# Performance work log

Hardware: AMD Instinct MI355X
Metric: run time of the kernel (lower is better)

Reference implementation:

```python
import jax, jax.numpy as jnp
import numpy as np
from jax import lax

MAX_INT = 10000.0
V, T0, E, H = 100000, 20, 256, 256
T = T0 + 2          # tagset_size + 2 (start = T-2, stop = T-1)
B, S = 32, 512
H2 = H // 2


def setup_inputs() -> dict:
    key = jax.random.key(0)
    ks = jax.random.split(key, 18)
    sd = 0.08
    trans = jax.random.normal(ks[0], (T, T), jnp.float32)
    trans = trans.at[-2, :].set(-MAX_INT).at[:, -1].set(-MAX_INT)
    return {
        "X": jax.random.randint(ks[1], (B, S), 0, V, jnp.int64),
        "Y": jax.random.randint(ks[2], (B, S), 0, T0, jnp.int64),
        "emb": jax.random.normal(ks[3], (V, E), jnp.float32) * sd,
        "Wih_f": jax.random.normal(ks[4], (4 * H2, E), jnp.float32) * sd,
        "Whh_f": jax.random.normal(ks[5], (4 * H2, H2), jnp.float32) * sd,
        "bih_f": jax.random.normal(ks[6], (4 * H2,), jnp.float32) * sd,
        "bhh_f": jax.random.normal(ks[7], (4 * H2,), jnp.float32) * sd,
        "Wih_b": jax.random.normal(ks[8], (4 * H2, E), jnp.float32) * sd,
        "Whh_b": jax.random.normal(ks[9], (4 * H2, H2), jnp.float32) * sd,
        "bih_b": jax.random.normal(ks[10], (4 * H2,), jnp.float32) * sd,
        "bhh_b": jax.random.normal(ks[11], (4 * H2,), jnp.float32) * sd,
        "fcW": jax.random.normal(ks[12], (T, H), jnp.float32) * sd,
        "fcb": jax.random.normal(ks[13], (T,), jnp.float32) * sd,
        "trans": trans,
        # original draws random (h0, c0) of shape (2, seq_len, H//2) each call
        "h0": jax.random.normal(ks[14], (2, S, H2), jnp.float32),
        "c0": jax.random.normal(ks[15], (2, S, H2), jnp.float32),
    }


def _lstm_dir(x, h0, c0, Wih, Whh, bih, bhh, reverse):
    # x: [B, S, E]; scans over axis 0 (as torch LSTM with batch_first=False does here)
    def step(carry, xt):
        h, c = carry
        g = xt @ Wih.T + bih + h @ Whh.T + bhh          # [S, 4*H2]
        i, f, gg, o = jnp.split(g, 4, axis=-1)
        c2 = jax.nn.sigmoid(f) * c + jax.nn.sigmoid(i) * jnp.tanh(gg)
        h2 = jax.nn.sigmoid(o) * jnp.tanh(c2)
        return (h2, c2), h2
    xs = x[::-1] if reverse else x
    _, hs = lax.scan(step, (h0, c0), xs)
    return hs[::-1] if reverse else hs                  # [B, S, H2]


def _feats(X, emb, Wih_f, Whh_f, bih_f, bhh_f, Wih_b, Whh_b, bih_b, bhh_b,
           fcW, fcb, h0, c0):
    e = emb[X]                                           # [B, S, E]
    hf = _lstm_dir(e, h0[0], c0[0], Wih_f, Whh_f, bih_f, bhh_f, False)
    hb = _lstm_dir(e, h0[1], c0[1], Wih_b, Whh_b, bih_b, bhh_b, True)
    lstm_out = jnp.concatenate([hf, hb], axis=-1)        # [B, S, H]
    return lstm_out @ fcW.T + fcb                        # [B, S, T]


def _crf_loss(feats, Y, trans):
    # forward algorithm (log partition), vectorized over batch
    alpha0 = jnp.full((B, T), -MAX_INT, feats.dtype).at[:, -2].set(0.0)

    def step(alpha, feat_t):                             # feat_t: [B, T]
        # alpha_new[b, next] = LSE_prev(alpha[b,prev] + trans[next,prev]) + feat[b,next]
        new = jax.nn.logsumexp(alpha[:, None, :] + trans[None, :, :], axis=2) + feat_t
        return new, None

    alpha, _ = lax.scan(step, alpha0, jnp.swapaxes(feats, 0, 1))
    forward_score = jax.nn.logsumexp(alpha + trans[-1][None, :], axis=1).mean()

    # gold score
    start = jnp.full((B, 1), T - 2, Y.dtype)
    tags = jnp.concatenate([start, Y], axis=1)           # [B, S+1]
    emit = jnp.take_along_axis(feats, Y[..., None], axis=2)[..., 0].sum(axis=1)
    trans_sc = trans[tags[:, 1:], tags[:, :-1]].sum(axis=1) + trans[-1, tags[:, -1]]
    gold_score = (emit + trans_sc).mean()
    return forward_score - gold_score


def reference(X, Y, emb, Wih_f, Whh_f, bih_f, bhh_f, Wih_b, Whh_b, bih_b, bhh_b,
              fcW, fcb, trans, h0, c0):
    feats = _feats(X, emb, Wih_f, Whh_f, bih_f, bhh_f, Wih_b, Whh_b, bih_b, bhh_b,
                   fcW, fcb, h0, c0)
    score = _crf_loss(feats, Y, trans)
    return score, Y
```

## Files before the change

### kernel.cpp

```cpp
#include <hip/hip_runtime.h>
#include <hip/hip_bf16.h>
#include <stdint.h>

typedef __attribute__((ext_vector_type(8))) short short8;
typedef __attribute__((ext_vector_type(4))) float f32x4;
typedef __attribute__((ext_vector_type(4))) unsigned short ushort4v;

#define NB 32
#define NS 512
#define NE 256
#define NH2 128
#define NG 512
#define NT 22

__device__ __forceinline__ unsigned short f2bf(float f) {
    union { float f; unsigned u; } v; v.f = f;
    unsigned r = v.u + 0x7fffu + ((v.u >> 16) & 1u);
    return (unsigned short)(r >> 16);
}
__device__ __forceinline__ float bf2f(unsigned short b) {
    union { unsigned u; float f; } v; v.u = ((unsigned)b) << 16;
    return v.f;
}
__device__ __forceinline__ float sigmoidf_(float x) {
    return __builtin_amdgcn_rcpf(1.f + __expf(-x));
}
__device__ __forceinline__ float tanhf_(float x) {
    return 1.f - 2.f * __builtin_amdgcn_rcpf(__expf(2.f * x) + 1.f);
}
__device__ __forceinline__ void wg_barrier() {
    __builtin_amdgcn_sched_barrier(0);
    asm volatile("s_waitcnt lgkmcnt(0)" ::: "memory");
    __builtin_amdgcn_s_barrier();
    __builtin_amdgcn_sched_barrier(0);
}
#define GL16(gsrc, ldst)                                                              \
    __builtin_amdgcn_global_load_lds(                                                 \
        (const __attribute__((address_space(1))) unsigned int*)(gsrc),                \
        (__attribute__((address_space(3))) unsigned int*)(ldst), 16, 0, 0)

__global__ void k_pre(const int* X, const float* emb, const int* Y,
                      const float* Wih_f, const float* Wih_b,
                      const float* Whh_f, const float* Whh_b, const float* fcW,
                      unsigned short* ebf, unsigned short* Wb_ih,
                      unsigned short* Wb_hh, unsigned short* fcpad, float* out)
{
    int idx = blockIdx.x * blockDim.x + threadIdx.x;
    const int nEmb = NB * NS * 64;
    if (idx < nEmb) {
        int r = idx >> 6, lane = idx & 63;
        int xr = X[r];
        f32x4 v = *(const f32x4*)(emb + (size_t)xr * NE + lane * 4);
        ushort4v o;
        o[0] = f2bf(v[0]); o[1] = f2bf(v[1]); o[2] = f2bf(v[2]); o[3] = f2bf(v[3]);
        *(ushort4v*)(ebf + (size_t)r * NE + lane * 4) = o;
        return;
    }
    int j = idx - nEmb;
    const int n1 = 2 * NG * NE;
    const int n2 = 2 * NG * NH2;
    const int n3 = 2 * 32 * NH2;
    const int n4 = NB * NS;
    if (j < n1) {
        const float* src = (j < NG * NE) ? Wih_f : Wih_b;
        Wb_ih[j] = f2bf(src[j % (NG * NE)]);
    } else if (j < n1 + n2) {
        int i2 = j - n1;
        const float* src = (i2 < NG * NH2) ? Whh_f : Whh_b;
        Wb_hh[i2] = f2bf(src[i2 % (NG * NH2)]);
    } else if (j < n1 + n2 + n3) {
        int i3 = j - n1 - n2;
        int d = i3 / (32 * NH2);
        int jj = (i3 / NH2) % 32;
        int k = i3 % NH2;
        fcpad[i3] = (jj < NT) ? f2bf(fcW[jj * 256 + d * NH2 + k]) : (unsigned short)0;
    } else if (j < n1 + n2 + n3 + n4) {
        int i4 = j - n1 - n2 - n3;
        out[1 + i4] = (float)Y[i4];
    }
}

__launch_bounds__(256)
__global__ void k_xproj(const unsigned short* ebf, const unsigned short* Wb_ih,
                        const float* bih_f, const float* bhh_f,
                        const float* bih_b, const float* bhh_b,
                        unsigned short* Xp)
{
    __shared__ __align__(16) unsigned short Atile[128 * 64];
    __shared__ __align__(16) unsigned short Btile[128 * 64];
    int dir = blockIdx.z;
    int r0 = blockIdx.x * 128;
    int g0 = blockIdx.y * 128;
    int tid = threadIdx.x;
    int w = tid >> 6, lane = tid & 63;
    int wr = w >> 1, wc = w & 1;
    int lrow = lane & 15, kg = lane >> 4;
    int srow8 = lane >> 3, schunk = lane & 7;
    const float* bih = dir ? bih_b : bih_f;
    const float* bhh = dir ? bhh_b : bhh_f;
    const unsigned short* Bsrc = Wb_ih + ((size_t)dir * NG + g0) * NE;
    const unsigned short* Asrc = ebf + (size_t)r0 * NE;

    f32x4 acc[4][4] = {};
#pragma unroll
    for (int ks = 0; ks < 4; ++ks) {
        int k0 = ks * 64;
#pragma unroll
        for (int i = 0; i < 4; ++i) {
            int rr = (w * 4 + i) * 8 + srow8;
            GL16(Asrc + (size_t)rr * NE + k0 + schunk * 8, Atile + (w * 4 + i) * 512);
            GL16(Bsrc + (size_t)rr * NE + k0 + schunk * 8, Btile + (w * 4 + i) * 512);
        }
        __syncthreads();
        short8 a[4][2], b[4][2];
#pragma unroll
        for (int mi = 0; mi < 4; ++mi)
#pragma unroll
            for (int kk = 0; kk < 2; ++kk)
                a[mi][kk] = *(const short8*)&Atile[(wr * 64 + mi * 16 + lrow) * 64 + kk * 32 + kg * 8];
#pragma unroll
        for (int ni = 0; ni < 4; ++ni)
#pragma unroll
            for (int kk = 0; kk < 2; ++kk)
                b[ni][kk] = *(const short8*)&Btile[(wc * 64 + ni * 16 + lrow) * 64 + kk * 32 + kg * 8];
#pragma unroll
        for (int mi = 0; mi < 4; ++mi)
#pragma unroll
            for (int ni = 0; ni < 4; ++ni)
#pragma unroll
                for (int kk = 0; kk < 2; ++kk)
                    acc[mi][ni] = __builtin_amdgcn_mfma_f32_16x16x32_bf16(a[mi][kk], b[ni][kk], acc[mi][ni], 0, 0, 0);
        __syncthreads();
    }

#pragma unroll
    for (int ni = 0; ni < 4; ++ni) {
        int g = g0 + wc * 64 + ni * 16 + lrow;
        float bias = bih[g] + bhh[g];
#pragma unroll
        for (int mi = 0; mi < 4; ++mi) {
            int r = r0 + wr * 64 + mi * 16 + kg * 4;
            int t = r >> 9;
            int s = r & 511;
            int sb = s >> 4;
            unsigned short* dst = Xp + ((((size_t)dir * 32 + sb) * 32 + t) << 13) + g * 16 + (s & 15);
            unsigned o0 = f2bf(acc[mi][ni][0] + bias);
            unsigned o1 = f2bf(acc[mi][ni][1] + bias);
            unsigned o2 = f2bf(acc[mi][ni][2] + bias);
            unsigned o3 = f2bf(acc[mi][ni][3] + bias);
            uint2 pk; pk.x = o0 | (o1 << 16); pk.y = o2 | (o3 << 16);
            *(uint2*)dst = pk;
        }
    }
}

__launch_bounds__(512, 2)
__global__ void k_lstm(const unsigned short* Wb_hh, const unsigned short* Xp,
                       unsigned short* Hout, const float* h0, const float* c0)
{
    __shared__ unsigned short h_lds[2][16 * 136];
    int dir = blockIdx.x >> 5;
    int sb = blockIdx.x & 31;
    int s0 = sb * 16;
    int tid = threadIdx.x;
    int w = tid >> 6, lane = tid & 63;
    int lrow = lane & 15, kg = lane >> 4;

    short8 bfr[4][4];
#pragma unroll
    for (int q = 0; q < 4; ++q) {
        const unsigned short* p = Wb_hh + ((size_t)dir * NG + (q * 128 + w * 16 + lrow)) * NH2 + kg * 8;
#pragma unroll
        for (int kf = 0; kf < 4; ++kf)
            bfr[q][kf] = *(const short8*)(p + kf * 32);
    }

    float c[4];
#pragma unroll
    for (int i = 0; i < 4; ++i)
        c[i] = c0[((size_t)dir * NS + s0 + kg * 4 + i) * NH2 + w * 16 + lrow];
    {
        int sl = tid >> 5, hq = tid & 31;
        f32x4 hv = *(const f32x4*)(h0 + ((size_t)dir * NS + s0 + sl) * NH2 + hq * 4);
        ushort4v hb; hb[0] = f2bf(hv[0]); hb[1] = f2bf(hv[1]); hb[2] = f2bf(hv[2]); hb[3] = f2bf(hv[3]);
        *(ushort4v*)&h_lds[0][sl * 136 + hq * 4] = hb;
    }

    const unsigned short* xbase = Xp + (((size_t)dir * 32 + sb) * 32) * 8192;
    unsigned short* hslot = Hout + (((size_t)dir * 32 + sb) * 32) * 2048;
    int xoff0 = (w * 16 + lrow) * 16 + kg * 4;

    ushort4v xA[4], xB[4];
#pragma unroll
    for (int q = 0; q < 4; ++q)
        xA[q] = *(const ushort4v*)(xbase + (size_t)(dir ? 31 : 0) * 8192 + xoff0 + q * 2048);
#pragma unroll
    for (int q = 0; q < 4; ++q)
        xB[q] = *(const ushort4v*)(xbase + (size_t)(dir ? 30 : 1) * 8192 + xoff0 + q * 2048);
    __syncthreads();

#define LSTM_STEP(T, XV, PR, PW)                                                       \
    {                                                                                  \
        int tx = dir ? 31 - (T) : (T);                                                 \
        short8 afr[4];                                                                 \
        _Pragma("unroll")                                                              \
        for (int kf = 0; kf < 4; ++kf)                                                 \
            afr[kf] = *(const short8*)&h_lds[PR][lrow * 136 + kf * 32 + kg * 8];       \
        f32x4 acc[4] = {};                                                             \
        _Pragma("unroll")                                                              \
        for (int q = 0; q < 4; ++q)                                                    \
            _Pragma("unroll")                                                          \
            for (int kf = 0; kf < 4; ++kf)                                             \
                acc[q] = __builtin_amdgcn_mfma_f32_16x16x32_bf16(afr[kf], bfr[q][kf],  \
                                                                 acc[q], 0, 0, 0);     \
        float gs[4][4];                                                                \
        _Pragma("unroll")                                                              \
        for (int q = 0; q < 4; ++q)                                                    \
            _Pragma("unroll")                                                          \
            for (int i = 0; i < 4; ++i)                                                \
                gs[q][i] = acc[q][i] + bf2f(XV[q][i]);                                 \
        if ((T) + 2 < 32) {                                                            \
            int txn = dir ? 29 - (T) : (T) + 2;                                        \
            _Pragma("unroll")                                                          \
            for (int q = 0; q < 4; ++q)                                                \
                XV[q] = *(const ushort4v*)(xbase + (size_t)txn * 8192 + xoff0 + q * 2048); \
        }                                                                              \
        _Pragma("unroll")                                                              \
        for (int i = 0; i < 4; ++i) {                                                  \
            float ci = sigmoidf_(gs[1][i]) * c[i] + sigmoidf_(gs[0][i]) * tanhf_(gs[2][i]); \
            c[i] = ci;                                                                 \
            unsigned short hb = f2bf(sigmoidf_(gs[3][i]) * tanhf_(ci));                \
            h_lds[PW][(kg * 4 + i) * 136 + w * 16 + lrow] = hb;                        \
            hslot[(size_t)tx * 2048 + (kg * 4 + i) * 128 + w * 16 + lrow] = hb;        \
        }                                                                              \
        wg_barrier();                                                                  \
    }

    for (int tt = 0; tt < 16; ++tt) {
        LSTM_STEP(2 * tt,     xA, ((2 * tt) & 1),     (((2 * tt) & 1) ^ 1))
        LSTM_STEP(2 * tt + 1, xB, ((2 * tt + 1) & 1), (((2 * tt + 1) & 1) ^ 1))
    }
#undef LSTM_STEP
}

__device__ __forceinline__ float mm_combine(const unsigned short* Rb, const unsigned short* Tb,
                                            int lane, f32x4 c[2][2])
{
    int lrow = lane & 15, kg = lane >> 4;
    short8 a0 = *(const short8*)(Rb + lrow * 32 + kg * 8);
    short8 a1 = *(const short8*)(Rb + (16 + lrow) * 32 + kg * 8);
    short8 b0 = *(const short8*)(Tb + lrow * 32 + kg * 8);
    short8 b1 = *(const short8*)(Tb + (16 + lrow) * 32 + kg * 8);
    c[0][0] = __builtin_amdgcn_mfma_f32_16x16x32_bf16(a0, b0, c[0][0], 0, 0, 0);
    c[0][1] = __builtin_amdgcn_mfma_f32_16x16x32_bf16(a0, b1, c[0][1], 0, 0, 0);
    c[1][0] = __builtin_amdgcn_mfma_f32_16x16x32_bf16(a1, b0, c[1][0], 0, 0, 0);
    c[1][1] = __builtin_amdgcn_mfma_f32_16x16x32_bf16(a1, b1, c[1][1], 0, 0, 0);
    float mx = 0.f;
#pragma unroll
    for (int ti = 0; ti < 2; ++ti)
#pragma unroll
        for (int tj = 0; tj < 2; ++tj)
#pragma unroll
            for (int i = 0; i < 4; ++i) mx = fmaxf(mx, c[ti][tj][i]);
#pragma unroll
    for (int off = 32; off; off >>= 1) mx = fmaxf(mx, __shfl_xor(mx, off));
    return fmaxf(mx, 1e-30f);
}

__device__ __forceinline__ void write_scaled(unsigned short* outp, bool Rlayout,
                                             int lane, const f32x4 c[2][2], float inv)
{
    int lrow = lane & 15, kg = lane >> 4;
    if (Rlayout) {
#pragma unroll
        for (int ti = 0; ti < 2; ++ti)
#pragma unroll
            for (int tj = 0; tj < 2; ++tj) {
                int cc = tj * 16 + lrow;
#pragma unroll
                for (int i = 0; i < 4; ++i) {
                    int r = ti * 16 + kg * 4 + i;
                    float v = (r < NT && cc < NT) ? c[ti][tj][i] * inv : 0.f;
                    outp[r * 32 + cc] = f2bf(v);
                }
            }
    } else {
#pragma unroll
        for (int ti = 0; ti < 2; ++ti)
#pragma unroll
            for (int tj = 0; tj < 2; ++tj) {
                int cc = tj * 16 + lrow;
                int r0 = ti * 16 + kg * 4;
                ushort4v pk;
#pragma unroll
                for (int i = 0; i < 4; ++i) {
                    int r = r0 + i;
                    float v = (r < NT && cc < NT) ? c[ti][tj][i] * inv : 0.f;
                    pk[i] = f2bf(v);
                }
                *(ushort4v*)(outp + cc * 32 + r0) = pk;
            }
    }
}

__launch_bounds__(256)
__global__ void k_fcrf(const unsigned short* Hout, const unsigned short* fcpad,
                       const float* fcb, const float* trans,
                       float* feats, unsigned short* Mseg, float* lscseg)
{
    __shared__ unsigned short mats[16 * 1024];
    __shared__ float etR[484], etT[484];
    __shared__ float ef[16 * 24];
    __shared__ float lscm[16];
    __shared__ f32x4 part[2][64];
    int b = blockIdx.x, seg = blockIdx.y;
    int tid = threadIdx.x;
    int w = tid >> 6, lane = tid & 63;
    int lrow = lane & 15, kg = lane >> 4;

    f32x4 fa[2] = {};
    if (w < 2) {
        int dir = w;
        const unsigned short* hb = Hout + (((size_t)dir * 32 + seg) * 32 + b) * 2048 + lrow * 128 + kg * 8;
        const unsigned short* fb = fcpad + dir * 4096 + lrow * 128 + kg * 8;
#pragma unroll
        for (int kf = 0; kf < 4; ++kf) {
            short8 a  = *(const short8*)(hb + kf * 32);
            short8 b0 = *(const short8*)(fb + kf * 32);
            short8 b1 = *(const short8*)(fb + 2048 + kf * 32);
            fa[0] = __builtin_amdgcn_mfma_f32_16x16x32_bf16(a, b0, fa[0], 0, 0, 0);
            fa[1] = __builtin_amdgcn_mfma_f32_16x16x32_bf16(a, b1, fa[1], 0, 0, 0);
        }
        if (dir == 1) { part[0][lane] = fa[0]; part[1][lane] = fa[1]; }
        if (w == 1 && lane < 16) lscm[lane] = 0.f;
    } else {
        for (int i = tid - 128; i < 484; i += 128) {
            float e = __expf(trans[i]);
            etR[i] = e;
            etT[(i % NT) * NT + (i / NT)] = e;
        }
    }
    __syncthreads();
    if (w == 0) {
        fa[0] += part[0][lane];
        fa[1] += part[1][lane];
#pragma unroll
        for (int nf = 0; nf < 2; ++nf) {
            int tag = nf * 16 + lrow;
            if (tag < NT) {
                float bias = fcb[tag];
#pragma unroll
                for (int i = 0; i < 4; ++i) {
                    int s = kg * 4 + i;
                    float f = fa[nf][i] + bias;
                    feats[((size_t)b * NS + seg * 16 + s) * NT + tag] = f;
                    ef[s * 24 + tag] = __expf(f);
                }
            }
        }
    }
    __syncthreads();

    for (int idx = tid; idx < 16 * 1024; idx += 256) {
        int t = idx >> 10, cell = idx & 1023, row = cell >> 5, col = cell & 31;
        float v = 0.f;
        if (row < NT && col < NT) {
            v = (t & 1) ? etR[row * NT + col] * ef[t * 24 + row]
                        : etT[row * NT + col] * ef[t * 24 + col];
        }
        mats[idx] = f2bf(v);
    }
    __syncthreads();

    for (int lvl = 0; lvl < 4; ++lvl) {
        int nP = 8 >> lvl;
        for (int p = w; p < nP; p += 4) {
            int aslot = (2 * p) << lvl, bslot = (2 * p + 1) << lvl;
            f32x4 c[2][2] = {};
            float mx = mm_combine(mats + bslot * 1024, mats + aslot * 1024, lane, c);
            float inv = __builtin_amdgcn_rcpf(mx);
            float nlsc = lscm[aslot] + lscm[bslot] + __logf(mx);
            if (lvl < 3) {
                write_scaled(mats + aslot * 1024, (p & 1) != 0, lane, c, inv);
                if (lane == 0) lscm[aslot] = nlsc;
            } else {
                write_scaled(Mseg + ((size_t)b * 32 + seg) * 1024, (seg & 1) != 0, lane, c, inv);
                if (lane == 0) lscseg[b * 32 + seg] = nlsc;
            }
        }
        __syncthreads();
    }
}

__launch_bounds__(256)
__global__ void k_crf2(const unsigned short* Mseg, const float* lscseg,
                       const float* feats, const float* trans, const int* Y,
                       float* fwd_sc, float* gold_sc)
{
    __shared__ unsigned short mats[16 * 1024];
    __shared__ float lscm[16];
    __shared__ float tl[484];
    __shared__ float col20[32];
    __shared__ float red[4];
    int b = blockIdx.x;
    int tid = threadIdx.x;
    int w = tid >> 6, lane = tid & 63;
    int lrow = lane & 15, kg = lane >> 4;

    for (int i = tid; i < 484; i += 256) tl[i] = trans[i];
    __syncthreads();

    const unsigned short* base = Mseg + (size_t)b * 32 * 1024;
    for (int p = w; p < 16; p += 4) {
        f32x4 c[2][2] = {};
        float mx = mm_combine(base + (2 * p + 1) * 1024, base + (2 * p) * 1024, lane, c);
        float inv = __builtin_amdgcn_rcpf(mx);
        float nlsc = lscseg[b * 32 + 2 * p] + lscseg[b * 32 + 2 * p + 1] + __logf(mx);
        write_scaled(mats + p * 1024, (p & 1) != 0, lane, c, inv);
        if (lane == 0) lscm[p] = nlsc;
    }
    __syncthreads();

    for (int lvl = 0; lvl < 4; ++lvl) {
        int nP = 8 >> lvl;
        for (int p = w; p < nP; p += 4) {
            int aslot = (2 * p) << lvl, bslot = (2 * p + 1) << lvl;
            f32x4 c[2][2] = {};
            float mx = mm_combine(mats + bslot * 1024, mats + aslot * 1024, lane, c);
            if (lvl < 3) {
                float inv = __builtin_amdgcn_rcpf(mx);
                float nlsc = lscm[aslot] + lscm[bslot] + __logf(mx);
                write_scaled(mats + aslot * 1024, (p & 1) != 0, lane, c, inv);
                if (lane == 0) lscm[aslot] = nlsc;
            } else {
                if (lrow == 4) {
#pragma unroll
                    for (int ti = 0; ti < 2; ++ti)
#pragma unroll
                        for (int i = 0; i < 4; ++i)
                            col20[ti * 16 + kg * 4 + i] = c[ti][1][i];
                }
                if (lane == 0) lscm[0] = lscm[0] + lscm[8];
            }
        }
        __syncthreads();
    }

    if (w == 0) {
        float v = 0.f;
        if (lane < NT) v = __expf(tl[(NT - 1) * NT + lane]) * col20[lane];
#pragma unroll
        for (int off = 32; off; off >>= 1) v += __shfl_xor(v, off);
        if (lane == 0) fwd_sc[b] = __logf(v) + lscm[0];
    }

    const float* fb = feats + (size_t)b * NS * NT;
    float acc = 0.f;
    for (int s = tid; s < NS; s += 256) {
        int y = Y[b * NS + s];
        int yp = s ? Y[b * NS + s - 1] : (NT - 2);
        acc += fb[s * NT + y] + tl[y * NT + yp];
    }
    if (tid == 0) acc += tl[(NT - 1) * NT + Y[b * NS + NS - 1]];
#pragma unroll
    for (int off = 32; off; off >>= 1) acc += __shfl_xor(acc, off);
    if (lane == 0) red[w] = acc;
    __syncthreads();
    if (tid == 0) gold_sc[b] = red[0] + red[1] + red[2] + red[3];
}

__global__ void k_final(const float* fwd_sc, const float* gold_sc, float* out)
{
    float v = (threadIdx.x < NB) ? (fwd_sc[threadIdx.x] - gold_sc[threadIdx.x]) : 0.f;
#pragma unroll
    for (int off = 32; off; off >>= 1) v += __shfl_xor(v, off);
    if (threadIdx.x == 0) out[0] = v * (1.f / NB);
}

extern "C" void kernel_launch(void* const* d_in, const int* in_sizes, int n_in,
                              void* d_out, int out_size, void* d_ws, size_t ws_size,
                              hipStream_t stream)
{
    const int* X = (const int*)d_in[0];
    const int* Y = (const int*)d_in[1];
    const float* emb = (const float*)d_in[2];
    const float* Wih_f = (const float*)d_in[3];
    const float* Whh_f = (const float*)d_in[4];
    const float* bih_f = (const float*)d_in[5];
    const float* bhh_f = (const float*)d_in[6];
    const float* Wih_b = (const float*)d_in[7];
    const float* Whh_b = (const float*)d_in[8];
    const float* bih_b = (const float*)d_in[9];
    const float* bhh_b = (const float*)d_in[10];
    const float* fcW = (const float*)d_in[11];
    const float* fcb = (const float*)d_in[12];
    const float* trans = (const float*)d_in[13];
    const float* h0 = (const float*)d_in[14];
    const float* c0 = (const float*)d_in[15];
    float* out = (float*)d_out;

    char* ws = (char*)d_ws;
    unsigned short* Wb_ih = (unsigned short*)(ws + 0);
    unsigned short* Wb_hh = (unsigned short*)(ws + 524288);
    unsigned short* fcpad = (unsigned short*)(ws + 786432);
    unsigned short* Xp    = (unsigned short*)(ws + 802816);
    float* feats          = (float*)(ws + 34357248);
    float* fwd_sc         = (float*)(ws + 35799040);
    float* gold_sc        = (float*)(ws + 35799168);
    unsigned short* ebf   = (unsigned short*)(ws + 35799296);
    unsigned short* Mseg  = ebf;
    float* lscseg         = (float*)(ws + 35799296 + 2097152);
    unsigned short* Hout  = (unsigned short*)(ws + 44187904);

    k_pre<<<dim3(5728), dim3(256), 0, stream>>>(X, emb, Y, Wih_f, Wih_b, Whh_f, Whh_b,
                                                fcW, ebf, Wb_ih, Wb_hh, fcpad, out);
    k_xproj<<<dim3(128, 4, 2), dim3(256), 0, stream>>>(ebf, Wb_ih, bih_f, bhh_f, bih_b, bhh_b, Xp);
    k_lstm<<<dim3(64), dim3(512), 0, stream>>>(Wb_hh, Xp, Hout, h0, c0);
    k_fcrf<<<dim3(32, 32), dim3(256), 0, stream>>>(Hout, fcpad, fcb, trans, feats, Mseg, lscseg);
    k_crf2<<<dim3(NB), dim3(256), 0, stream>>>(Mseg, lscseg, feats, trans, Y, fwd_sc, gold_sc);
    k_final<<<dim3(1), dim3(64), 0, stream>>>(fwd_sc, gold_sc, out);
    (void)in_sizes; (void)n_in; (void)out_size; (void)ws_size;
}
```

Measured before the change: 97.65 us.

## Fuse FC projection into LSTM recurrence and double-buffer input projection GEMM

The LSTM kernel now computes the FC tag projection of each previous hidden state with extra MFMAs inside the recurrence and stages per-direction partial features in LDS. It then writes them out instead of storing the full hidden sequence to global memory. The FC/CRF kernel sums the two direction partials plus bias and computes per-segment gold-score partials, so k_crf2 only reduces them. The xproj GEMM gains double-buffered LDS tiles with explicit waitcnt/barrier scheduling to overlap loads with MFMA. The cost is extra MFMA and LDS work on the serial LSTM critical path for two of the waves.

```diff
diff --git a/kernel.cpp b/kernel.cpp
--- a/kernel.cpp
+++ b/kernel.cpp
@@ -86,8 +86,8 @@
                         const float* bih_b, const float* bhh_b,
                         unsigned short* Xp)
 {
-    __shared__ __align__(16) unsigned short Atile[128 * 64];
-    __shared__ __align__(16) unsigned short Btile[128 * 64];
+    __shared__ __align__(16) unsigned short Atile[2][128 * 64];
+    __shared__ __align__(16) unsigned short Btile[2][128 * 64];
     int dir = blockIdx.z;
     int r0 = blockIdx.x * 128;
     int g0 = blockIdx.y * 128;
@@ -101,28 +101,42 @@
     const unsigned short* Bsrc = Wb_ih + ((size_t)dir * NG + g0) * NE;
     const unsigned short* Asrc = ebf + (size_t)r0 * NE;
 
+#define STAGE(bufi, ks)                                                                \
+    do {                                                                               \
+        int k0_ = (ks) * 64;                                                           \
+        _Pragma("unroll")                                                              \
+        for (int i_ = 0; i_ < 4; ++i_) {                                               \
+            int rr_ = (w * 4 + i_) * 8 + srow8;                                        \
+            GL16(Asrc + (size_t)rr_ * NE + k0_ + schunk * 8, &Atile[bufi][(w * 4 + i_) * 512]); \
+            GL16(Bsrc + (size_t)rr_ * NE + k0_ + schunk * 8, &Btile[bufi][(w * 4 + i_) * 512]); \
+        }                                                                              \
+    } while (0)
+
+    STAGE(0, 0);
     f32x4 acc[4][4] = {};
 #pragma unroll
     for (int ks = 0; ks < 4; ++ks) {
-        int k0 = ks * 64;
-#pragma unroll
-        for (int i = 0; i < 4; ++i) {
-            int rr = (w * 4 + i) * 8 + srow8;
-            GL16(Asrc + (size_t)rr * NE + k0 + schunk * 8, Atile + (w * 4 + i) * 512);
-            GL16(Bsrc + (size_t)rr * NE + k0 + schunk * 8, Btile + (w * 4 + i) * 512);
+        const int cur = ks & 1;
+        if (ks < 3) {
+            STAGE(cur ^ 1, ks + 1);
+            asm volatile("s_waitcnt vmcnt(8)" ::: "memory");
+        } else {
+            asm volatile("s_waitcnt vmcnt(0)" ::: "memory");
         }
-        __syncthreads();
+        __builtin_amdgcn_sched_barrier(0);
+        __builtin_amdgcn_s_barrier();
+        __builtin_amdgcn_sched_barrier(0);
         short8 a[4][2], b[4][2];
 #pragma unroll
         for (int mi = 0; mi < 4; ++mi)
 #pragma unroll
             for (int kk = 0; kk < 2; ++kk)
-                a[mi][kk] = *(const short8*)&Atile[(wr * 64 + mi * 16 + lrow) * 64 + kk * 32 + kg * 8];
+                a[mi][kk] = *(const short8*)&Atile[cur][(wr * 64 + mi * 16 + lrow) * 64 + kk * 32 + kg * 8];
 #pragma unroll
         for (int ni = 0; ni < 4; ++ni)
 #pragma unroll
             for (int kk = 0; kk < 2; ++kk)
-                b[ni][kk] = *(const short8*)&Btile[(wc * 64 + ni * 16 + lrow) * 64 + kk * 32 + kg * 8];
+                b[ni][kk] = *(const short8*)&Btile[cur][(wc * 64 + ni * 16 + lrow) * 64 + kk * 32 + kg * 8];
 #pragma unroll
         for (int mi = 0; mi < 4; ++mi)
 #pragma unroll
@@ -130,8 +144,12 @@
 #pragma unroll
                 for (int kk = 0; kk < 2; ++kk)
                     acc[mi][ni] = __builtin_amdgcn_mfma_f32_16x16x32_bf16(a[mi][kk], b[ni][kk], acc[mi][ni], 0, 0, 0);
-        __syncthreads();
-    }
+        asm volatile("s_waitcnt lgkmcnt(0)" ::: "memory");
+        __builtin_amdgcn_sched_barrier(0);
+        __builtin_amdgcn_s_barrier();
+        __builtin_amdgcn_sched_barrier(0);
+    }
+#undef STAGE
 
 #pragma unroll
     for (int ni = 0; ni < 4; ++ni) {
@@ -155,10 +173,12 @@
 }
 
 __launch_bounds__(512, 2)
-__global__ void k_lstm(const unsigned short* Wb_hh, const unsigned short* Xp,
-                       unsigned short* Hout, const float* h0, const float* c0)
+__global__ void k_lstm(const unsigned short* Wb_hh, const unsigned short* fcpad,
+                       const unsigned short* Xp, const float* h0, const float* c0,
+                       float* featsP)
 {
     __shared__ unsigned short h_lds[2][16 * 136];
+    __shared__ float featsL[32 * 16 * 24];
     int dir = blockIdx.x >> 5;
     int sb = blockIdx.x & 31;
     int s0 = sb * 16;
@@ -173,6 +193,13 @@
 #pragma unroll
         for (int kf = 0; kf < 4; ++kf)
             bfr[q][kf] = *(const short8*)(p + kf * 32);
+    }
+    short8 fcfr[4];
+    if (w < 2) {
+        const unsigned short* p = fcpad + ((size_t)dir * 32 + (w * 16 + lrow)) * NH2 + kg * 8;
+#pragma unroll
+        for (int kf = 0; kf < 4; ++kf)
+            fcfr[kf] = *(const short8*)(p + kf * 32);
     }
 
     float c[4];
@@ -187,9 +214,7 @@
     }
 
     const unsigned short* xbase = Xp + (((size_t)dir * 32 + sb) * 32) * 8192;
-    unsigned short* hslot = Hout + (((size_t)dir * 32 + sb) * 32) * 2048;
     int xoff0 = (w * 16 + lrow) * 16 + kg * 4;
-
     ushort4v xA[4], xB[4];
 #pragma unroll
     for (int q = 0; q < 4; ++q)
@@ -201,7 +226,6 @@
 
 #define LSTM_STEP(T, XV, PR, PW)                                                       \
     {                                                                                  \
-        int tx = dir ? 31 - (T) : (T);                                                 \
         short8 afr[4];                                                                 \
         _Pragma("unroll")                                                              \
         for (int kf = 0; kf < 4; ++kf)                                                 \
@@ -213,6 +237,19 @@
             for (int kf = 0; kf < 4; ++kf)                                             \
                 acc[q] = __builtin_amdgcn_mfma_f32_16x16x32_bf16(afr[kf], bfr[q][kf],  \
                                                                  acc[q], 0, 0, 0);     \
+        if (w < 2 && (T) > 0) {                     \
+            int txp = dir ? 32 - (T) : (T) - 1;                                        \
+            f32x4 fa = {};                                                             \
+            _Pragma("unroll")                                                          \
+            for (int kf = 0; kf < 4; ++kf)                                             \
+                fa = __builtin_amdgcn_mfma_f32_16x16x32_bf16(afr[kf], fcfr[kf], fa, 0, 0, 0); \
+            int tag = w * 16 + lrow;                                                   \
+            if (tag < NT) {                                                            \
+                _Pragma("unroll")                                                      \
+                for (int i = 0; i < 4; ++i)                                            \
+                    featsL[(txp * 16 + kg * 4 + i) * 24 + tag] = fa[i];                \
+            }                                                                          \
+        }                                                                              \
         float gs[4][4];                                                                \
         _Pragma("unroll")                                                              \
         for (int q = 0; q < 4; ++q)                                                    \
@@ -229,9 +266,7 @@
         for (int i = 0; i < 4; ++i) {                                                  \
             float ci = sigmoidf_(gs[1][i]) * c[i] + sigmoidf_(gs[0][i]) * tanhf_(gs[2][i]); \
             c[i] = ci;                                                                 \
-            unsigned short hb = f2bf(sigmoidf_(gs[3][i]) * tanhf_(ci));                \
-            h_lds[PW][(kg * 4 + i) * 136 + w * 16 + lrow] = hb;                        \
-            hslot[(size_t)tx * 2048 + (kg * 4 + i) * 128 + w * 16 + lrow] = hb;        \
+            h_lds[PW][(kg * 4 + i) * 136 + w * 16 + lrow] = f2bf(sigmoidf_(gs[3][i]) * tanhf_(ci)); \
         }                                                                              \
         wg_barrier();                                                                  \
     }
@@ -241,6 +276,31 @@
         LSTM_STEP(2 * tt + 1, xB, ((2 * tt + 1) & 1), (((2 * tt + 1) & 1) ^ 1))
     }
 #undef LSTM_STEP
+
+    if (w < 2) {
+        short8 afr[4];
+#pragma unroll
+        for (int kf = 0; kf < 4; ++kf)
+            afr[kf] = *(const short8*)&h_lds[0][lrow * 136 + kf * 32 + kg * 8];
+        f32x4 fa = {};
+#pragma unroll
+        for (int kf = 0; kf < 4; ++kf)
+            fa = __builtin_amdgcn_mfma_f32_16x16x32_bf16(afr[kf], fcfr[kf], fa, 0, 0, 0);
+        int txl = dir ? 0 : 31;
+        int tag = w * 16 + lrow;
+        if (tag < NT) {
+#pragma unroll
+            for (int i = 0; i < 4; ++i)
+                featsL[(txl * 16 + kg * 4 + i) * 24 + tag] = fa[i];
+        }
+    }
+    __syncthreads();
+    int ftx = tid >> 4, fs = tid & 15;
+    float* gdst = featsP + (((size_t)dir * 32 + ftx) * 512 + s0 + fs) * 24;
+    const float* lsrc = featsL + (ftx * 16 + fs) * 24;
+#pragma unroll
+    for (int j = 0; j < 6; ++j)
+        ((f32x4*)gdst)[j] = ((const f32x4*)lsrc)[j];
 }
 
 __device__ __forceinline__ float mm_combine(const unsigned short* Rb, const unsigned short* Tb,
@@ -304,62 +364,42 @@
 }
 
 __launch_bounds__(256)
-__global__ void k_fcrf(const unsigned short* Hout, const unsigned short* fcpad,
-                       const float* fcb, const float* trans,
-                       float* feats, unsigned short* Mseg, float* lscseg)
+__global__ void k_fcrf(const float* featsP, const float* fcb, const float* trans,
+                       const int* Y, unsigned short* Mseg, float* lscseg, float* goldp)
 {
     __shared__ unsigned short mats[16 * 1024];
     __shared__ float etR[484], etT[484];
     __shared__ float ef[16 * 24];
+    __shared__ float fl[16 * 24];
     __shared__ float lscm[16];
-    __shared__ f32x4 part[2][64];
     int b = blockIdx.x, seg = blockIdx.y;
     int tid = threadIdx.x;
     int w = tid >> 6, lane = tid & 63;
-    int lrow = lane & 15, kg = lane >> 4;
-
-    f32x4 fa[2] = {};
-    if (w < 2) {
-        int dir = w;
-        const unsigned short* hb = Hout + (((size_t)dir * 32 + seg) * 32 + b) * 2048 + lrow * 128 + kg * 8;
-        const unsigned short* fb = fcpad + dir * 4096 + lrow * 128 + kg * 8;
-#pragma unroll
-        for (int kf = 0; kf < 4; ++kf) {
-            short8 a  = *(const short8*)(hb + kf * 32);
-            short8 b0 = *(const short8*)(fb + kf * 32);
-            short8 b1 = *(const short8*)(fb + 2048 + kf * 32);
-            fa[0] = __builtin_amdgcn_mfma_f32_16x16x32_bf16(a, b0, fa[0], 0, 0, 0);
-            fa[1] = __builtin_amdgcn_mfma_f32_16x16x32_bf16(a, b1, fa[1], 0, 0, 0);
-        }
-        if (dir == 1) { part[0][lane] = fa[0]; part[1][lane] = fa[1]; }
-        if (w == 1 && lane < 16) lscm[lane] = 0.f;
-    } else {
-        for (int i = tid - 128; i < 484; i += 128) {
-            float e = __expf(trans[i]);
-            etR[i] = e;
-            etT[(i % NT) * NT + (i / NT)] = e;
-        }
-    }
+
+    for (int i = tid; i < 484; i += 256) {
+        float e = __expf(trans[i]);
+        etR[i] = e;
+        etT[(i % NT) * NT + (i / NT)] = e;
+    }
+    for (int i = tid; i < 16 * NT; i += 256) {
+        int s = i / NT, j = i % NT;
+        size_t base = ((size_t)b * 512 + seg * 16 + s) * 24 + j;
+        float f = featsP[base] + featsP[(size_t)32 * 512 * 24 + base] + fcb[j];
+        fl[s * 24 + j] = f;
+        ef[s * 24 + j] = __expf(f);
+    }
+    if (tid < 16) lscm[tid] = 0.f;
     __syncthreads();
-    if (w == 0) {
-        fa[0] += part[0][lane];
-        fa[1] += part[1][lane];
-#pragma unroll
-        for (int nf = 0; nf < 2; ++nf) {
-            int tag = nf * 16 + lrow;
-            if (tag < NT) {
-                float bias = fcb[tag];
-#pragma unroll
-                for (int i = 0; i < 4; ++i) {
-                    int s = kg * 4 + i;
-                    float f = fa[nf][i] + bias;
-                    feats[((size_t)b * NS + seg * 16 + s) * NT + tag] = f;
-                    ef[s * 24 + tag] = __expf(f);
-                }
-            }
-        }
-    }
-    __syncthreads();
+
+    if (w == 3 && lane < 16) {
+        int sg = seg * 16 + lane;
+        int y = Y[b * NS + sg];
+        int yp = sg ? Y[b * NS + sg - 1] : (NT - 2);
+        float gp = fl[lane * 24 + y] + trans[y * NT + yp];
+#pragma unroll
+        for (int off = 8; off; off >>= 1) gp += __shfl_xor(gp, off);
+        if (lane == 0) goldp[b * 32 + seg] = gp;
+    }
 
     for (int idx = tid; idx < 16 * 1024; idx += 256) {
         int t = idx >> 10, cell = idx & 1023, row = cell >> 5, col = cell & 31;
@@ -394,14 +434,13 @@
 
 __launch_bounds__(256)
 __global__ void k_crf2(const unsigned short* Mseg, const float* lscseg,
-                       const float* feats, const float* trans, const int* Y,
+                       const float* trans, const int* Y, const float* goldp,
                        float* fwd_sc, float* gold_sc)
 {
     __shared__ unsigned short mats[16 * 1024];
     __shared__ float lscm[16];
     __shared__ float tl[484];
     __shared__ float col20[32];
-    __shared__ float red[4];
     int b = blockIdx.x;
     int tid = threadIdx.x;
     int w = tid >> 6, lane = tid & 63;
@@ -453,20 +492,12 @@
         for (int off = 32; off; off >>= 1) v += __shfl_xor(v, off);
         if (lane == 0) fwd_sc[b] = __logf(v) + lscm[0];
     }
-
-    const float* fb = feats + (size_t)b * NS * NT;
-    float acc = 0.f;
-    for (int s = tid; s < NS; s += 256) {
-        int y = Y[b * NS + s];
-        int yp = s ? Y[b * NS + s - 1] : (NT - 2);
-        acc += fb[s * NT + y] + tl[y * NT + yp];
-    }
-    if (tid == 0) acc += tl[(NT - 1) * NT + Y[b * NS + NS - 1]];
-#pragma unroll
-    for (int off = 32; off; off >>= 1) acc += __shfl_xor(acc, off);
-    if (lane == 0) red[w] = acc;
-    __syncthreads();
-    if (tid == 0) gold_sc[b] = red[0] + red[1] + red[2] + red[3];
+    if (w == 1) {
+        float g = (lane < 32) ? goldp[b * 32 + lane] : 0.f;
+#pragma unroll
+        for (int off = 16; off; off >>= 1) g += __shfl_xor(g, off);
+        if (lane == 0) gold_sc[b] = g + tl[(NT - 1) * NT + Y[b * NS + NS - 1]];
+    }
 }
 
 __global__ void k_final(const float* fwd_sc, const float* gold_sc, float* out)
@@ -504,20 +535,20 @@
     unsigned short* Wb_hh = (unsigned short*)(ws + 524288);
     unsigned short* fcpad = (unsigned short*)(ws + 786432);
     unsigned short* Xp    = (unsigned short*)(ws + 802816);
-    float* feats          = (float*)(ws + 34357248);
-    float* fwd_sc         = (float*)(ws + 35799040);
-    float* gold_sc        = (float*)(ws + 35799168);
-    unsigned short* ebf   = (unsigned short*)(ws + 35799296);
+    float* featsP         = (float*)(ws + 34357248);
+    float* goldp          = (float*)(ws + 37502976);
+    float* fwd_sc         = (float*)(ws + 37507072);
+    float* gold_sc        = (float*)(ws + 37507200);
+    unsigned short* ebf   = (unsigned short*)(ws + 37507328);
     unsigned short* Mseg  = ebf;
-    float* lscseg         = (float*)(ws + 35799296 + 2097152);
-    unsigned short* Hout  = (unsigned short*)(ws + 44187904);
+    float* lscseg         = (float*)(ws + 45895936);
 
     k_pre<<<dim3(5728), dim3(256), 0, stream>>>(X, emb, Y, Wih_f, Wih_b, Whh_f, Whh_b,
                                                 fcW, ebf, Wb_ih, Wb_hh, fcpad, out);
     k_xproj<<<dim3(128, 4, 2), dim3(256), 0, stream>>>(ebf, Wb_ih, bih_f, bhh_f, bih_b, bhh_b, Xp);
-    k_lstm<<<dim3(64), dim3(512), 0, stream>>>(Wb_hh, Xp, Hout, h0, c0);
-    k_fcrf<<<dim3(32, 32), dim3(256), 0, stream>>>(Hout, fcpad, fcb, trans, feats, Mseg, lscseg);
-    k_crf2<<<dim3(NB), dim3(256), 0, stream>>>(Mseg, lscseg, feats, trans, Y, fwd_sc, gold_sc);
+    k_lstm<<<dim3(64), dim3(512), 0, stream>>>(Wb_hh, fcpad, Xp, h0, c0, featsP);
+    k_fcrf<<<dim3(32, 32), dim3(256), 0, stream>>>(featsP, fcb, trans, Y, Mseg, lscseg, goldp);
+    k_crf2<<<dim3(NB), dim3(256), 0, stream>>>(Mseg, lscseg, trans, Y, goldp, fwd_sc, gold_sc);
     k_final<<<dim3(1), dim3(64), 0, stream>>>(fwd_sc, gold_sc, out);
     (void)in_sizes; (void)n_in; (void)out_size; (void)ws_size;
 }
```

Measured after the change: 97.98 us. Within noise of the previous version (+0.3%).
